# Performance work log

Hardware: AMD Instinct MI355X
Metric: run time of the kernel (lower is better)

## Reference

```python
import jax, jax.numpy as jnp
import numpy as np

T, N, E = 12, 100000, 3200000
F = H = 64
O, L = 32, 2


def setup_inputs() -> dict:
    key = jax.random.key(0)
    ks = jax.random.split(key, 13)
    sc = 0.08  # keep gate pre-activations in a sane range
    return {
        "x": jax.random.normal(ks[0], (T, N, F), jnp.float32),
        "hidden_states": jax.random.normal(ks[1], (L, N, H), jnp.float32),
        "cell_states": jax.random.normal(ks[2], (L, N, H), jnp.float32),
        "Wx_self": jax.random.normal(ks[3], (L, 4, F, H), jnp.float32) * sc,
        "Wx_neigh": jax.random.normal(ks[4], (L, 4, F, H), jnp.float32) * sc,
        "Wh_self": jax.random.normal(ks[5], (L, 4, H, H), jnp.float32) * sc,
        "Wh_neigh": jax.random.normal(ks[6], (L, 4, H, H), jnp.float32) * sc,
        "w_c": jax.random.normal(ks[7], (L, 3, H), jnp.float32) * sc,  # peephole i,f,o
        "bias": jax.random.normal(ks[8], (L, 4, H), jnp.float32) * sc,  # i,f,c,o
        "Wout": jax.random.normal(ks[9], (H, O), jnp.float32) * sc,
        "bout": jax.random.normal(ks[10], (O,), jnp.float32) * sc,
        "src": jax.random.randint(ks[11], (E,), 0, N, jnp.int32),
        "dst": jax.random.randint(ks[12], (E,), 0, N, jnp.int32),
    }


def reference(x, hidden_states, cell_states, Wx_self, Wx_neigh, Wh_self,
              Wh_neigh, w_c, bias, Wout, bout, src, dst):
    # mean aggregation over incoming edges (DGL copy_u + mean reduce)
    deg = jax.ops.segment_sum(jnp.ones((E,), x.dtype), dst, num_segments=N)
    deg_inv = jnp.where(deg > 0, 1.0 / deg, 0.0)[:, None]  # [N,1]

    def mean_agg(feat):  # [N,D] -> [N,D]
        return jax.ops.segment_sum(feat[src], dst, num_segments=N) * deg_inv

    def gates(feat, agg, Ws, Wn):  # Ws,Wn: [4,D,H] -> [4,N,H]
        return (jnp.einsum('nf,gfh->gnh', feat, Ws)
                + jnp.einsum('nf,gfh->gnh', agg, Wn))

    def step(carry, x_t):
        hs, cs = carry  # [L,N,H] each
        inp = x_t
        new_h, new_c = [], []
        for j in range(L):
            h, c = hs[j], cs[j]
            x_agg = mean_agg(inp)  # reuse_msg_passing: one agg shared by 4 gates
            h_agg = mean_agg(h)
            pre = gates(inp, x_agg, Wx_self[j], Wx_neigh[j]) \
                + gates(h, h_agg, Wh_self[j], Wh_neigh[j])  # [4,N,H]
            i = jax.nn.sigmoid(pre[0] + w_c[j, 0] * c + bias[j, 0])
            f = jax.nn.sigmoid(pre[1] + w_c[j, 1] * c + bias[j, 1])
            c_tilde = jnp.tanh(pre[2] + bias[j, 2])
            nc = f * c + i * c_tilde
            o = jax.nn.sigmoid(pre[3] + w_c[j, 2] * nc + bias[j, 3])
            nh = o * jnp.tanh(nc)
            new_h.append(nh)
            new_c.append(nc)
            inp = nh
        out_t = inp @ Wout + bout  # [N,O]
        return (jnp.stack(new_h), jnp.stack(new_c)), out_t

    (h_f, c_f), outs = jax.lax.scan(step, (hidden_states, cell_states), x)
    return outs, h_f, c_f  # outs: [T,N,O]
```

## Files before the change

### kernel.cpp

```cpp
#include <hip/hip_runtime.h>

#define T_STEPS 12
#define NN 100000
#define EE 3200000
#define HD 64
#define OD 32
#define NBK 391

typedef __attribute__((ext_vector_type(8))) short short8;
typedef __attribute__((ext_vector_type(4))) float f32x4;
typedef __attribute__((ext_vector_type(2))) float f32x2;
typedef unsigned short u16;
typedef unsigned char u8;

__device__ __forceinline__ u16 f2b(float x) {
  union { float f; unsigned u; } v; v.f = x;
  unsigned r = v.u + 0x7FFFu + ((v.u >> 16) & 1u);
  return (u16)(r >> 16);
}
__device__ __forceinline__ float sigm(float x) {
  x = fminf(fmaxf(x, -30.f), 30.f);
  return 1.0f / (1.0f + __expf(-x));
}
__device__ __forceinline__ float tanh_f(float x) {
  x = fminf(fmaxf(x, -15.f), 15.f);
  float e = __expf(2.0f * x);
  return (e - 1.0f) / (e + 1.0f);
}

__device__ __forceinline__ uint2 pack8_fp8(const float* f) {
  unsigned lo = 0, hi = 0;
  lo = __builtin_amdgcn_cvt_pk_fp8_f32(f[0], f[1], lo, false);
  lo = __builtin_amdgcn_cvt_pk_fp8_f32(f[2], f[3], lo, true);
  hi = __builtin_amdgcn_cvt_pk_fp8_f32(f[4], f[5], hi, false);
  hi = __builtin_amdgcn_cvt_pk_fp8_f32(f[6], f[7], hi, true);
  return make_uint2(lo, hi);
}
__device__ __forceinline__ u8 f2q(float x) {
  return (u8)(__builtin_amdgcn_cvt_pk_fp8_f32(x, 0.f, 0u, false) & 0xFFu);
}
__device__ __forceinline__ void acc8_fp8(uint2 v, float* a) {
  f32x2 p0 = __builtin_amdgcn_cvt_pk_f32_fp8(v.x, false);
  f32x2 p1 = __builtin_amdgcn_cvt_pk_f32_fp8(v.x, true);
  f32x2 p2 = __builtin_amdgcn_cvt_pk_f32_fp8(v.y, false);
  f32x2 p3 = __builtin_amdgcn_cvt_pk_f32_fp8(v.y, true);
  a[0] += p0[0]; a[1] += p0[1]; a[2] += p1[0]; a[3] += p1[1];
  a[4] += p2[0]; a[5] += p2[1]; a[6] += p3[0]; a[7] += p3[1];
}
__device__ __forceinline__ void dec16_acc(uint4 q, float* a) {
  f32x2 t;
  t = __builtin_amdgcn_cvt_pk_f32_fp8(q.x, false); a[0] += t[0]; a[1] += t[1];
  t = __builtin_amdgcn_cvt_pk_f32_fp8(q.x, true);  a[2] += t[0]; a[3] += t[1];
  t = __builtin_amdgcn_cvt_pk_f32_fp8(q.y, false); a[4] += t[0]; a[5] += t[1];
  t = __builtin_amdgcn_cvt_pk_f32_fp8(q.y, true);  a[6] += t[0]; a[7] += t[1];
  t = __builtin_amdgcn_cvt_pk_f32_fp8(q.z, false); a[8] += t[0]; a[9] += t[1];
  t = __builtin_amdgcn_cvt_pk_f32_fp8(q.z, true);  a[10] += t[0]; a[11] += t[1];
  t = __builtin_amdgcn_cvt_pk_f32_fp8(q.w, false); a[12] += t[0]; a[13] += t[1];
  t = __builtin_amdgcn_cvt_pk_f32_fp8(q.w, true);  a[14] += t[0]; a[15] += t[1];
}
__device__ __forceinline__ short8 s8_from_fp8(uint2 q) {
  f32x2 p0 = __builtin_amdgcn_cvt_pk_f32_fp8(q.x, false);
  f32x2 p1 = __builtin_amdgcn_cvt_pk_f32_fp8(q.x, true);
  f32x2 p2 = __builtin_amdgcn_cvt_pk_f32_fp8(q.y, false);
  f32x2 p3 = __builtin_amdgcn_cvt_pk_f32_fp8(q.y, true);
  short8 o;
  o[0] = (short)f2b(p0[0]); o[1] = (short)f2b(p0[1]);
  o[2] = (short)f2b(p1[0]); o[3] = (short)f2b(p1[1]);
  o[4] = (short)f2b(p2[0]); o[5] = (short)f2b(p2[1]);
  o[6] = (short)f2b(p3[0]); o[7] = (short)f2b(p3[1]);
  return o;
}
__device__ __forceinline__ short8 s8_from_f32(float4 a, float4 b) {
  short8 o;
  o[0] = (short)f2b(a.x); o[1] = (short)f2b(a.y);
  o[2] = (short)f2b(a.z); o[3] = (short)f2b(a.w);
  o[4] = (short)f2b(b.x); o[5] = (short)f2b(b.y);
  o[6] = (short)f2b(b.z); o[7] = (short)f2b(b.w);
  return o;
}

__global__ __launch_bounds__(256) void k_bhist(const int* __restrict__ dst,
                                               int* __restrict__ bcnt, int E) {
  __shared__ int h[NBK];
  for (int i = threadIdx.x; i < NBK; i += 256) h[i] = 0;
  __syncthreads();
  int base = blockIdx.x * 4096;
#pragma unroll
  for (int i = 0; i < 16; ++i) {
    int e = base + i * 256 + threadIdx.x;
    if (e < E) atomicAdd(&h[dst[e] >> 8], 1);
  }
  __syncthreads();
  for (int i = threadIdx.x; i < NBK; i += 256)
    if (h[i]) atomicAdd(&bcnt[i], h[i]);
}

__global__ __launch_bounds__(512) void k_bscan(const int* __restrict__ bcnt,
                                               int* __restrict__ bcur) {
  __shared__ int buf[512];
  int tid = threadIdx.x;
  int v = (tid < NBK) ? bcnt[tid] : 0;
  buf[tid] = v;
  __syncthreads();
  for (int off = 1; off < 512; off <<= 1) {
    int t = (tid >= off) ? buf[tid - off] : 0;
    __syncthreads();
    buf[tid] += t;
    __syncthreads();
  }
  if (tid < NBK) bcur[tid] = buf[tid] - v;
}

__global__ __launch_bounds__(256) void k_bscatter(const int* __restrict__ src,
                                                  const int* __restrict__ dst,
                                                  int* __restrict__ bcur,
                                                  uint2* __restrict__ binned, int E) {
  __shared__ int h[NBK];
  __shared__ int base[NBK];
  __shared__ int cur[NBK];
  for (int i = threadIdx.x; i < NBK; i += 256) { h[i] = 0; cur[i] = 0; }
  __syncthreads();
  int b0 = blockIdx.x * 4096;
  int d[16], s[16];
#pragma unroll
  for (int i = 0; i < 16; ++i) {
    int e = b0 + i * 256 + threadIdx.x;
    if (e < E) {
      d[i] = dst[e];
      s[i] = src[e];
      atomicAdd(&h[d[i] >> 8], 1);
    } else d[i] = -1;
  }
  __syncthreads();
  for (int i = threadIdx.x; i < NBK; i += 256)
    if (h[i]) base[i] = atomicAdd(&bcur[i], h[i]);
  __syncthreads();
#pragma unroll
  for (int i = 0; i < 16; ++i) {
    if (d[i] >= 0) {
      int bk = d[i] >> 8;
      int r = atomicAdd(&cur[bk], 1);
      binned[base[bk] + r] = make_uint2((unsigned)s[i], (unsigned)d[i]);
    }
  }
}

__global__ __launch_bounds__(256) void k_count2(const uint2* __restrict__ binned,
                                                int* __restrict__ deg, int E) {
  int e = blockIdx.x * 256 + threadIdx.x;
  if (e < E) atomicAdd(&deg[binned[e].y], 1);
}

__global__ __launch_bounds__(1024) void k_scanA(const int* __restrict__ deg,
                                                int* __restrict__ excl,
                                                int* __restrict__ btot, int n) {
  __shared__ int buf[1024];
  int tid = threadIdx.x;
  int i = blockIdx.x * 1024 + tid;
  int v = (i < n) ? deg[i] : 0;
  buf[tid] = v;
  __syncthreads();
  for (int off = 1; off < 1024; off <<= 1) {
    int t = (tid >= off) ? buf[tid - off] : 0;
    __syncthreads();
    buf[tid] += t;
    __syncthreads();
  }
  if (i < n) excl[i] = buf[tid] - v;
  if (tid == 1023) btot[blockIdx.x] = buf[1023];
}

__global__ __launch_bounds__(128) void k_scanB(const int* __restrict__ btot,
                                               int* __restrict__ boffs, int nb) {
  __shared__ int buf[128];
  int tid = threadIdx.x;
  int v = (tid < nb) ? btot[tid] : 0;
  buf[tid] = v;
  __syncthreads();
  for (int off = 1; off < 128; off <<= 1) {
    int t = (tid >= off) ? buf[tid - off] : 0;
    __syncthreads();
    buf[tid] += t;
    __syncthreads();
  }
  if (tid < nb) boffs[tid] = buf[tid] - v;
}

__global__ __launch_bounds__(1024) void k_scanC(const int* __restrict__ deg,
                                                const int* __restrict__ excl,
                                                const int* __restrict__ boffs,
                                                int* __restrict__ row_ptr,
                                                int* __restrict__ cursor,
                                                float* __restrict__ deg_inv, int n) {
  int i = blockIdx.x * 1024 + threadIdx.x;
  if (i < n) {
    int v = excl[i] + boffs[blockIdx.x];
    int d = deg[i];
    row_ptr[i] = v;
    cursor[i] = v;
    deg_inv[i] = d ? (1.0f / (float)d) : 0.0f;
    if (i == n - 1) row_ptr[n] = v + d;
  }
}

__global__ __launch_bounds__(256) void k_scatter2(const uint2* __restrict__ binned,
                                                  int* __restrict__ cursor,
                                                  int* __restrict__ csr, int E) {
  int e = blockIdx.x * 256 + threadIdx.x;
  if (e < E) {
    uint2 p = binned[e];
    int pos = atomicAdd(&cursor[p.y], 1);
    csr[pos] = (int)p.x;
  }
}

__global__ __launch_bounds__(256) void k_prep(const float* __restrict__ Wxs,
                                              const float* __restrict__ Wxn,
                                              const float* __restrict__ Whs,
                                              const float* __restrict__ Whn,
                                              u16* __restrict__ bprep) {
  int idx = blockIdx.x * 256 + threadIdx.x;
  int l = idx >> 16;
  int kb = (idx >> 13) & 7;
  int fi = (idx >> 9) & 15;
  int ln = (idx >> 3) & 63;
  int j = idx & 7;
  int fc = kb * 32 + ((ln >> 4) << 3) + j;
  int g = fi & 3;
  int kk = ((fi >> 2) << 4) + (ln & 15);
  int t = fc >> 6, f = fc & 63;
  const float* tabs[4] = {Wxs, Wxn, Whs, Whn};
  bprep[idx] = f2b(tabs[t][((size_t)(l * 4 + g) * 64 + f) * 64 + kk]);
}

__global__ __launch_bounds__(256) void k_prepw(const float* __restrict__ Wout,
                                               u16* __restrict__ wp) {
  int idx = blockIdx.x * 256 + threadIdx.x;
  int kb = idx >> 10;
  int fi = (idx >> 9) & 1;
  int ln = (idx >> 3) & 63;
  int j = idx & 7;
  int k = kb * 32 + ((ln >> 4) << 3) + j;
  int o = fi * 16 + (ln & 15);
  wp[idx] = f2b(Wout[k * 32 + o]);
}

__global__ __launch_bounds__(256) void k_convxall(const float* __restrict__ x,
                                                  u8* __restrict__ XQ) {
  int tid = blockIdx.x * 256 + threadIdx.x;
  int j = tid & 7;
  int tn = tid >> 3;
  int n = tn % NN;
  int t = tn / NN;
  const float* rp = x + (size_t)tn * 64 + j * 8;
  float4 v0 = *reinterpret_cast<const float4*>(rp);
  float4 v1 = *reinterpret_cast<const float4*>(rp + 4);
  float f[8] = {v0.x, v0.y, v0.z, v0.w, v1.x, v1.y, v1.z, v1.w};
  *reinterpret_cast<uint2*>(XQ + (size_t)n * 768 + t * 64 + j * 8) = pack8_fp8(f);
}

__global__ __launch_bounds__(256) void k_inith(const float* __restrict__ h0,
                                               u16* __restrict__ H0bf,
                                               u16* __restrict__ L1bf,
                                               u8* __restrict__ HQ) {
  int idx = blockIdx.x * 256 + threadIdx.x;
  int n = idx >> 3, j = idx & 7;
#pragma unroll
  for (int L = 0; L < 2; ++L) {
    const float* rp = h0 + (size_t)L * NN * 64 + (size_t)n * 64 + j * 8;
    float4 v0 = *reinterpret_cast<const float4*>(rp);
    float4 v1 = *reinterpret_cast<const float4*>(rp + 4);
    float f[8] = {v0.x, v0.y, v0.z, v0.w, v1.x, v1.y, v1.z, v1.w};
    short8 o;
#pragma unroll
    for (int i = 0; i < 8; ++i) o[i] = (short)f2b(f[i]);
    if (L == 0)
      *reinterpret_cast<short8*>(H0bf + (size_t)n * 64 + j * 8) = o;
    else
      *reinterpret_cast<short8*>(L1bf + (size_t)n * 64 + j * 8) = o;
    *reinterpret_cast<uint2*>(HQ + (size_t)n * 128 + L * 64 + j * 8) = pack8_fp8(f);
  }
}

__global__ __launch_bounds__(256) void k_aggx(const u8* __restrict__ XQ,
                                              const int* __restrict__ row_ptr,
                                              const int* __restrict__ csr,
                                              const float* __restrict__ deg_inv,
                                              u8* __restrict__ AGGXq) {
  int node = blockIdx.x * 4 + (threadIdx.x >> 6);
  int lane = threadIdx.x & 63;
  int g = lane >> 4, m = lane & 15;
  int start = row_ptr[node], end = row_ptr[node + 1];
  float acc[3][16];
#pragma unroll
  for (int p = 0; p < 3; ++p)
#pragma unroll
    for (int i = 0; i < 16; ++i) acc[p][i] = 0.f;
  int e = start + g;
  for (; e + 4 < end; e += 8) {
    int s0 = csr[e], s1 = csr[e + 4];
    const u8* r0 = XQ + (size_t)s0 * 768 + m * 16;
    const u8* r1 = XQ + (size_t)s1 * 768 + m * 16;
#pragma unroll
    for (int p = 0; p < 3; ++p) {
      uint4 q0 = *reinterpret_cast<const uint4*>(r0 + p * 256);
      uint4 q1 = *reinterpret_cast<const uint4*>(r1 + p * 256);
      dec16_acc(q0, acc[p]);
      dec16_acc(q1, acc[p]);
    }
  }
  if (e < end) {
    int s0 = csr[e];
    const u8* r0 = XQ + (size_t)s0 * 768 + m * 16;
#pragma unroll
    for (int p = 0; p < 3; ++p) {
      uint4 q0 = *reinterpret_cast<const uint4*>(r0 + p * 256);
      dec16_acc(q0, acc[p]);
    }
  }
#pragma unroll
  for (int off = 16; off < 64; off <<= 1)
#pragma unroll
    for (int p = 0; p < 3; ++p)
#pragma unroll
      for (int i = 0; i < 16; ++i) acc[p][i] += __shfl_xor(acc[p][i], off);
  if (g == 0) {
    float sc = deg_inv[node];
#pragma unroll
    for (int p = 0; p < 3; ++p) {
      float f[16];
#pragma unroll
      for (int i = 0; i < 16; ++i) f[i] = acc[p][i] * sc;
      uint4 o;
      unsigned w;
      w = 0; w = __builtin_amdgcn_cvt_pk_fp8_f32(f[0], f[1], w, false);
      w = __builtin_amdgcn_cvt_pk_fp8_f32(f[2], f[3], w, true); o.x = w;
      w = 0; w = __builtin_amdgcn_cvt_pk_fp8_f32(f[4], f[5], w, false);
      w = __builtin_amdgcn_cvt_pk_fp8_f32(f[6], f[7], w, true); o.y = w;
      w = 0; w = __builtin_amdgcn_cvt_pk_fp8_f32(f[8], f[9], w, false);
      w = __builtin_amdgcn_cvt_pk_fp8_f32(f[10], f[11], w, true); o.z = w;
      w = 0; w = __builtin_amdgcn_cvt_pk_fp8_f32(f[12], f[13], w, false);
      w = __builtin_amdgcn_cvt_pk_fp8_f32(f[14], f[15], w, true); o.w = w;
      int t = p * 4 + (m >> 2);
      *reinterpret_cast<uint4*>(AGGXq + ((size_t)t * NN + node) * 64 + (m & 3) * 16) = o;
    }
  }
}

__global__ __launch_bounds__(256) void k_agg_pair(const u8* __restrict__ Q,
                                                  const int* __restrict__ row_ptr,
                                                  const int* __restrict__ csr,
                                                  const float* __restrict__ deg_inv,
                                                  u16* __restrict__ outp) {
  int node = blockIdx.x * 4 + (threadIdx.x >> 6);
  int lane = threadIdx.x & 63;
  int g = lane >> 4, m = lane & 15;
  int start = row_ptr[node], end = row_ptr[node + 1];
  float a[8] = {0, 0, 0, 0, 0, 0, 0, 0};
  int e = start + g;
  for (; e + 12 < end; e += 16) {
    int s0 = csr[e], s1 = csr[e + 4], s2 = csr[e + 8], s3 = csr[e + 12];
    uint2 v0 = *reinterpret_cast<const uint2*>(Q + (size_t)s0 * 128 + m * 8);
    uint2 v1 = *reinterpret_cast<const uint2*>(Q + (size_t)s1 * 128 + m * 8);
    uint2 v2 = *reinterpret_cast<const uint2*>(Q + (size_t)s2 * 128 + m * 8);
    uint2 v3 = *reinterpret_cast<const uint2*>(Q + (size_t)s3 * 128 + m * 8);
    acc8_fp8(v0, a); acc8_fp8(v1, a); acc8_fp8(v2, a); acc8_fp8(v3, a);
  }
  if (e + 4 < end) {
    int s0 = csr[e], s1 = csr[e + 4];
    uint2 v0 = *reinterpret_cast<const uint2*>(Q + (size_t)s0 * 128 + m * 8);
    uint2 v1 = *reinterpret_cast<const uint2*>(Q + (size_t)s1 * 128 + m * 8);
    acc8_fp8(v0, a); acc8_fp8(v1, a);
    e += 8;
  }
  if (e < end) {
    int s0 = csr[e];
    uint2 v0 = *reinterpret_cast<const uint2*>(Q + (size_t)s0 * 128 + m * 8);
    acc8_fp8(v0, a);
  }
#pragma unroll
  for (int off = 16; off < 64; off <<= 1) {
#pragma unroll
    for (int i = 0; i < 8; ++i) a[i] += __shfl_xor(a[i], off);
  }
  if (g == 0) {
    float sc = deg_inv[node];
    short8 o;
#pragma unroll
    for (int i = 0; i < 8; ++i) o[i] = (short)f2b(a[i] * sc);
    *reinterpret_cast<short8*>(outp + (size_t)node * 128 + m * 8) = o;
  }
}

__global__ __launch_bounds__(256, 2) void k_gates0(
    const float* __restrict__ xin, const u8* __restrict__ aggxq,
    u16* __restrict__ h0bf, const u16* __restrict__ agghl,
    u8* __restrict__ hq, float* __restrict__ cst, float* __restrict__ hf32,
    const u16* __restrict__ bprepl,
    const float* __restrict__ wcl, const float* __restrict__ biasl,
    int n_nodes, int writef32) {
  const int tid = threadIdx.x;
  const int lane = tid & 63;
  const int w = tid >> 6;
  const int nb = blockIdx.x * 64;
  const int cl = lane & 15;
  const int kg = lane >> 4;

  short8 breg[8][4];
#pragma unroll
  for (int kb = 0; kb < 8; ++kb)
#pragma unroll
    for (int fl = 0; fl < 4; ++fl)
      breg[kb][fl] = *reinterpret_cast<const short8*>(
          bprepl + (kb << 13) + (((w << 2) + fl) << 9) + (lane << 3));

  int gnc[4];
#pragma unroll
  for (int rg = 0; rg < 4; ++rg) {
    int g = nb + rg * 16 + cl;
    gnc[rg] = (g < n_nodes) ? g : (n_nodes - 1);
  }

  f32x4 acc[4][4];
  f32x4 z4 = {0.f, 0.f, 0.f, 0.f};
#pragma unroll
  for (int a = 0; a < 4; ++a)
#pragma unroll
    for (int b = 0; b < 4; ++b) acc[a][b] = z4;

  const int koff = kg << 3;
#pragma unroll
  for (int kb = 0; kb < 8; ++kb) {
    const int idx = ((kb & 1) << 5) + koff;
#pragma unroll
    for (int rg = 0; rg < 4; ++rg) {
      short8 a;
      if (kb < 2) {
        const float* rp = xin + (size_t)gnc[rg] * 64 + idx;
        a = s8_from_f32(*reinterpret_cast<const float4*>(rp),
                        *reinterpret_cast<const float4*>(rp + 4));
      } else if (kb < 4) {
        a = s8_from_fp8(*reinterpret_cast<const uint2*>(aggxq + (size_t)gnc[rg] * 64 + idx));
      } else if (kb < 6) {
        a = *reinterpret_cast<const short8*>(h0bf + (size_t)gnc[rg] * 64 + idx);
      } else {
        a = *reinterpret_cast<const short8*>(agghl + (size_t)gnc[rg] * 128 + idx);
      }
      acc[rg][0] = __builtin_amdgcn_mfma_f32_16x16x32_bf16(a, breg[kb][0], acc[rg][0], 0, 0, 0);
      acc[rg][1] = __builtin_amdgcn_mfma_f32_16x16x32_bf16(a, breg[kb][1], acc[rg][1], 0, 0, 0);
      acc[rg][2] = __builtin_amdgcn_mfma_f32_16x16x32_bf16(a, breg[kb][2], acc[rg][2], 0, 0, 0);
      acc[rg][3] = __builtin_amdgcn_mfma_f32_16x16x32_bf16(a, breg[kb][3], acc[rg][3], 0, 0, 0);
    }
  }

  const int k = (w << 4) + cl;
  const float wci = wcl[k], wcf = wcl[64 + k], wco = wcl[128 + k];
  const float bi = biasl[k], bfg = biasl[64 + k], bc = biasl[128 + k], bo = biasl[192 + k];
#pragma unroll
  for (int rg = 0; rg < 4; ++rg) {
#pragma unroll
    for (int r = 0; r < 4; ++r) {
      int n = nb + rg * 16 + kg * 4 + r;
      if (n < n_nodes) {
        size_t off = (size_t)n * 64 + k;
        float c_old = cst[off];
        float ig = sigm(acc[rg][0][r] + wci * c_old + bi);
        float fg = sigm(acc[rg][1][r] + wcf * c_old + bfg);
        float ct = tanh_f(acc[rg][2][r] + bc);
        float nc = fg * c_old + ig * ct;
        float og = sigm(acc[rg][3][r] + wco * nc + bo);
        float nh = og * tanh_f(nc);
        cst[off] = nc;
        h0bf[off] = f2b(nh);
        hq[(size_t)n * 128 + k] = f2q(nh);
        if (writef32) hf32[off] = nh;
      }
    }
  }
}

__global__ __launch_bounds__(256, 2) void k_gates1(
    const u16* __restrict__ h0bf, const u16* __restrict__ agghl,
    u16* __restrict__ l1bf, u8* __restrict__ hq,
    float* __restrict__ cst, float* __restrict__ hf32,
    const u16* __restrict__ bprepl,
    const float* __restrict__ wcl, const float* __restrict__ biasl,
    const u16* __restrict__ wproj, const float* __restrict__ boutp,
    float* __restrict__ outp, int n_nodes, int writef32) {
  __shared__ u16 Hsm[64 * 64];
  const int tid = threadIdx.x;
  const int lane = tid & 63;
  const int w = tid >> 6;
  const int nb = blockIdx.x * 64;
  const int cl = lane & 15;
  const int kg = lane >> 4;

  short8 breg[8][4];
#pragma unroll
  for (int kb = 0; kb < 8; ++kb)
#pragma unroll
    for (int fl = 0; fl < 4; ++fl)
      breg[kb][fl] = *reinterpret_cast<const short8*>(
          bprepl + (kb << 13) + (((w << 2) + fl) << 9) + (lane << 3));

  int gnc[4];
#pragma unroll
  for (int rg = 0; rg < 4; ++rg) {
    int g = nb + rg * 16 + cl;
    gnc[rg] = (g < n_nodes) ? g : (n_nodes - 1);
  }

  f32x4 acc[4][4];
  f32x4 z4 = {0.f, 0.f, 0.f, 0.f};
#pragma unroll
  for (int a = 0; a < 4; ++a)
#pragma unroll
    for (int b = 0; b < 4; ++b) acc[a][b] = z4;

  const int koff = kg << 3;
#pragma unroll
  for (int kb = 0; kb < 8; ++kb) {
    const int idx = ((kb & 1) << 5) + koff;
#pragma unroll
    for (int rg = 0; rg < 4; ++rg) {
      short8 a;
      if (kb < 2) {
        a = *reinterpret_cast<const short8*>(h0bf + (size_t)gnc[rg] * 64 + idx);
      } else if (kb < 4) {
        a = *reinterpret_cast<const short8*>(agghl + (size_t)gnc[rg] * 128 + idx);
      } else if (kb < 6) {
        a = *reinterpret_cast<const short8*>(l1bf + (size_t)gnc[rg] * 64 + idx);
      } else {
        a = *reinterpret_cast<const short8*>(agghl + (size_t)gnc[rg] * 128 + 64 + idx);
      }
      acc[rg][0] = __builtin_amdgcn_mfma_f32_16x16x32_bf16(a, breg[kb][0], acc[rg][0], 0, 0, 0);
      acc[rg][1] = __builtin_amdgcn_mfma_f32_16x16x32_bf16(a, breg[kb][1], acc[rg][1], 0, 0, 0);
      acc[rg][2] = __builtin_amdgcn_mfma_f32_16x16x32_bf16(a, breg[kb][2], acc[rg][2], 0, 0, 0);
      acc[rg][3] = __builtin_amdgcn_mfma_f32_16x16x32_bf16(a, breg[kb][3], acc[rg][3], 0, 0, 0);
    }
  }

  const int k = (w << 4) + cl;
  const float wci = wcl[k], wcf = wcl[64 + k], wco = wcl[128 + k];
  const float bi = biasl[k], bfg = biasl[64 + k], bc = biasl[128 + k], bo = biasl[192 + k];
#pragma unroll
  for (int rg = 0; rg < 4; ++rg) {
#pragma unroll
    for (int r = 0; r < 4; ++r) {
      int n = nb + rg * 16 + kg * 4 + r;
      if (n < n_nodes) {
        size_t off = (size_t)n * 64 + k;
        float c_old = cst[off];
        float ig = sigm(acc[rg][0][r] + wci * c_old + bi);
        float fg = sigm(acc[rg][1][r] + wcf * c_old + bfg);
        float ct = tanh_f(acc[rg][2][r] + bc);
        float nc = fg * c_old + ig * ct;
        float og = sigm(acc[rg][3][r] + wco * nc + bo);
        float nh = og * tanh_f(nc);
        cst[off] = nc;
        u16 hb = f2b(nh);
        l1bf[off] = hb;
        hq[(size_t)n * 128 + 64 + k] = f2q(nh);
        Hsm[(rg * 16 + kg * 4 + r) * 64 + k] = hb;
        if (writef32) hf32[off] = nh;
      }
    }
  }

  __syncthreads();
  short8 bw[2][2];
#pragma unroll
  for (int kb = 0; kb < 2; ++kb)
#pragma unroll
    for (int fi = 0; fi < 2; ++fi)
      bw[kb][fi] = *reinterpret_cast<const short8*>(wproj + (((kb * 2 + fi) * 64 + lane) << 3));
  short8 a0 = *reinterpret_cast<const short8*>(&Hsm[(w * 16 + cl) * 64 + kg * 8]);
  short8 a1 = *reinterpret_cast<const short8*>(&Hsm[(w * 16 + cl) * 64 + 32 + kg * 8]);
  f32x4 p0 = z4, p1 = z4;
  p0 = __builtin_amdgcn_mfma_f32_16x16x32_bf16(a0, bw[0][0], p0, 0, 0, 0);
  p0 = __builtin_amdgcn_mfma_f32_16x16x32_bf16(a1, bw[1][0], p0, 0, 0, 0);
  p1 = __builtin_amdgcn_mfma_f32_16x16x32_bf16(a0, bw[0][1], p1, 0, 0, 0);
  p1 = __builtin_amdgcn_mfma_f32_16x16x32_bf16(a1, bw[1][1], p1, 0, 0, 0);
  const float bo0 = boutp[cl], bo1 = boutp[16 + cl];
#pragma unroll
  for (int r = 0; r < 4; ++r) {
    int n = nb + w * 16 + kg * 4 + r;
    if (n < n_nodes) {
      outp[(size_t)n * OD + cl] = p0[r] + bo0;
      outp[(size_t)n * OD + 16 + cl] = p1[r] + bo1;
    }
  }
}

extern "C" void kernel_launch(void* const* d_in, const int* in_sizes, int n_in,
                              void* d_out, int out_size, void* d_ws, size_t ws_size,
                              hipStream_t stream) {
  const float* x = (const float*)d_in[0];
  const float* h0 = (const float*)d_in[1];
  const float* c0 = (const float*)d_in[2];
  const float* Wxs = (const float*)d_in[3];
  const float* Wxn = (const float*)d_in[4];
  const float* Whs = (const float*)d_in[5];
  const float* Whn = (const float*)d_in[6];
  const float* wc = (const float*)d_in[7];
  const float* bias = (const float*)d_in[8];
  const float* Wout = (const float*)d_in[9];
  const float* bout = (const float*)d_in[10];
  const int* src = (const int*)d_in[11];
  const int* dst = (const int*)d_in[12];

  float* out = (float*)d_out;
  float* outs = out;
  float* hstate = out + (size_t)T_STEPS * NN * OD;
  float* cstate = hstate + (size_t)2 * NN * HD;

  char* p = (char*)d_ws;
  auto alloc = [&](size_t bytes) {
    char* r = p;
    p += (bytes + 255) & ~(size_t)255;
    return r;
  };
  int* csr = (int*)alloc((size_t)EE * 4);
  u8* XQ = (u8*)alloc((size_t)NN * 768);
  uint2* binned = (uint2*)XQ;
  u8* AGGXq = (u8*)alloc((size_t)T_STEPS * NN * 64);
  int* row_ptr = (int*)alloc((size_t)(NN + 1) * 4);
  int* cursor = (int*)alloc((size_t)NN * 4);
  int* deg = (int*)alloc((size_t)NN * 4);
  int* excl = (int*)alloc((size_t)NN * 4);
  int* btot = (int*)alloc(128 * 4);
  int* boffs = (int*)alloc(128 * 4);
  int* bcnt = (int*)alloc(NBK * 4);
  int* bcur = (int*)alloc(NBK * 4);
  float* deg_inv = (float*)alloc((size_t)NN * 4);
  u16* H0bf = (u16*)alloc((size_t)NN * 64 * 2);
  u16* L1bf = (u16*)alloc((size_t)NN * 64 * 2);
  u8* HQ = (u8*)alloc((size_t)NN * 128);
  u16* AGGHL = (u16*)alloc((size_t)NN * 128 * 2);
  u16* bprep = (u16*)alloc((size_t)2 * 65536 * 2);
  u16* wprep = (u16*)alloc((size_t)2048 * 2);

  const int nscan = (NN + 1023) / 1024;
  const int nchunk = (EE + 4095) / 4096;

  hipMemsetAsync(deg, 0, (size_t)NN * 4, stream);
  hipMemsetAsync(bcnt, 0, (size_t)NBK * 4, stream);
  k_bhist<<<nchunk, 256, 0, stream>>>(dst, bcnt, EE);
  k_bscan<<<1, 512, 0, stream>>>(bcnt, bcur);
  k_bscatter<<<nchunk, 256, 0, stream>>>(src, dst, bcur, binned, EE);
  k_count2<<<(EE + 255) / 256, 256, 0, stream>>>(binned, deg, EE);
  k_scanA<<<nscan, 1024, 0, stream>>>(deg, excl, btot, NN);
  k_scanB<<<1, 128, 0, stream>>>(btot, boffs, nscan);
  k_scanC<<<nscan, 1024, 0, stream>>>(deg, excl, boffs, row_ptr, cursor, deg_inv, NN);
  k_scatter2<<<(EE + 255) / 256, 256, 0, stream>>>(binned, cursor, csr, EE);
  k_prep<<<512, 256, 0, stream>>>(Wxs, Wxn, Whs, Whn, bprep);
  k_prepw<<<8, 256, 0, stream>>>(Wout, wprep);
  k_convxall<<<(T_STEPS * NN * 8 + 255) / 256, 256, 0, stream>>>(x, XQ);
  k_inith<<<NN * 8 / 256, 256, 0, stream>>>(h0, H0bf, L1bf, HQ);
  hipMemcpyAsync(cstate, c0, (size_t)2 * NN * HD * 4, hipMemcpyDeviceToDevice, stream);
  k_aggx<<<(NN + 3) / 4, 256, 0, stream>>>(XQ, row_ptr, csr, deg_inv, AGGXq);
  k_agg_pair<<<(NN + 3) / 4, 256, 0, stream>>>(HQ, row_ptr, csr, deg_inv, AGGHL);

  for (int t = 0; t < T_STEPS; ++t) {
    int wf = (t == T_STEPS - 1) ? 1 : 0;
    k_gates0<<<(NN + 63) / 64, 256, 0, stream>>>(
        x + (size_t)t * NN * HD, AGGXq + (size_t)t * NN * 64,
        H0bf, AGGHL, HQ, cstate, hstate, bprep, wc, bias, NN, wf);
    k_agg_pair<<<(NN + 3) / 4, 256, 0, stream>>>(HQ, row_ptr, csr, deg_inv, AGGHL);
    k_gates1<<<(NN + 63) / 64, 256, 0, stream>>>(
        H0bf, AGGHL, L1bf, HQ,
        cstate + (size_t)NN * HD, hstate + (size_t)NN * HD,
        bprep + 65536, wc + 192, bias + 256,
        wprep, bout, outs + (size_t)t * NN * OD, NN, wf);
  }
}
```

Before: 2.998 ms.

## Fuse layer-1 gates with next step's layer-0 gates; widen aggregation loads

Layer-1 gates for step t and layer-0 gates for step t+1 now run in one kernel, after a single pairwise aggregation per step. Layer 0 of step 0 is hoisted before the loop. This saves a launch per step, and the second half rereads the block's own h0 and aggregate rows while they are likely still cached. The pair-aggregation kernel now uses 16-byte fp8 loads with 8 lanes per row and packed f32x2 accumulation, to cut gather instruction count. The cost is higher register pressure in the fused kernel and extra barriers for shared-memory reuse.

```diff
diff --git a/kernel.cpp b/kernel.cpp
--- a/kernel.cpp
+++ b/kernel.cpp
@@ -39,24 +39,15 @@
 __device__ __forceinline__ u8 f2q(float x) {
   return (u8)(__builtin_amdgcn_cvt_pk_fp8_f32(x, 0.f, 0u, false) & 0xFFu);
 }
-__device__ __forceinline__ void acc8_fp8(uint2 v, float* a) {
-  f32x2 p0 = __builtin_amdgcn_cvt_pk_f32_fp8(v.x, false);
-  f32x2 p1 = __builtin_amdgcn_cvt_pk_f32_fp8(v.x, true);
-  f32x2 p2 = __builtin_amdgcn_cvt_pk_f32_fp8(v.y, false);
-  f32x2 p3 = __builtin_amdgcn_cvt_pk_f32_fp8(v.y, true);
-  a[0] += p0[0]; a[1] += p0[1]; a[2] += p1[0]; a[3] += p1[1];
-  a[4] += p2[0]; a[5] += p2[1]; a[6] += p3[0]; a[7] += p3[1];
-}
-__device__ __forceinline__ void dec16_acc(uint4 q, float* a) {
-  f32x2 t;
-  t = __builtin_amdgcn_cvt_pk_f32_fp8(q.x, false); a[0] += t[0]; a[1] += t[1];
-  t = __builtin_amdgcn_cvt_pk_f32_fp8(q.x, true);  a[2] += t[0]; a[3] += t[1];
-  t = __builtin_amdgcn_cvt_pk_f32_fp8(q.y, false); a[4] += t[0]; a[5] += t[1];
-  t = __builtin_amdgcn_cvt_pk_f32_fp8(q.y, true);  a[6] += t[0]; a[7] += t[1];
-  t = __builtin_amdgcn_cvt_pk_f32_fp8(q.z, false); a[8] += t[0]; a[9] += t[1];
-  t = __builtin_amdgcn_cvt_pk_f32_fp8(q.z, true);  a[10] += t[0]; a[11] += t[1];
-  t = __builtin_amdgcn_cvt_pk_f32_fp8(q.w, false); a[12] += t[0]; a[13] += t[1];
-  t = __builtin_amdgcn_cvt_pk_f32_fp8(q.w, true);  a[14] += t[0]; a[15] += t[1];
+__device__ __forceinline__ void dec16_acc2(uint4 q, f32x2* a) {
+  a[0] += __builtin_amdgcn_cvt_pk_f32_fp8(q.x, false);
+  a[1] += __builtin_amdgcn_cvt_pk_f32_fp8(q.x, true);
+  a[2] += __builtin_amdgcn_cvt_pk_f32_fp8(q.y, false);
+  a[3] += __builtin_amdgcn_cvt_pk_f32_fp8(q.y, true);
+  a[4] += __builtin_amdgcn_cvt_pk_f32_fp8(q.z, false);
+  a[5] += __builtin_amdgcn_cvt_pk_f32_fp8(q.z, true);
+  a[6] += __builtin_amdgcn_cvt_pk_f32_fp8(q.w, false);
+  a[7] += __builtin_amdgcn_cvt_pk_f32_fp8(q.w, true);
 }
 __device__ __forceinline__ short8 s8_from_fp8(uint2 q) {
   f32x2 p0 = __builtin_amdgcn_cvt_pk_f32_fp8(q.x, false);
@@ -291,11 +282,11 @@
   int lane = threadIdx.x & 63;
   int g = lane >> 4, m = lane & 15;
   int start = row_ptr[node], end = row_ptr[node + 1];
-  float acc[3][16];
+  f32x2 acc[3][8];
 #pragma unroll
   for (int p = 0; p < 3; ++p)
 #pragma unroll
-    for (int i = 0; i < 16; ++i) acc[p][i] = 0.f;
+    for (int i = 0; i < 8; ++i) acc[p][i] = (f32x2){0.f, 0.f};
   int e = start + g;
   for (; e + 4 < end; e += 8) {
     int s0 = csr[e], s1 = csr[e + 4];
@@ -305,8 +296,8 @@
     for (int p = 0; p < 3; ++p) {
       uint4 q0 = *reinterpret_cast<const uint4*>(r0 + p * 256);
       uint4 q1 = *reinterpret_cast<const uint4*>(r1 + p * 256);
-      dec16_acc(q0, acc[p]);
-      dec16_acc(q1, acc[p]);
+      dec16_acc2(q0, acc[p]);
+      dec16_acc2(q1, acc[p]);
     }
   }
   if (e < end) {
@@ -315,7 +306,7 @@
 #pragma unroll
     for (int p = 0; p < 3; ++p) {
       uint4 q0 = *reinterpret_cast<const uint4*>(r0 + p * 256);
-      dec16_acc(q0, acc[p]);
+      dec16_acc2(q0, acc[p]);
     }
   }
 #pragma unroll
@@ -323,14 +314,20 @@
 #pragma unroll
     for (int p = 0; p < 3; ++p)
 #pragma unroll
-      for (int i = 0; i < 16; ++i) acc[p][i] += __shfl_xor(acc[p][i], off);
+      for (int i = 0; i < 8; ++i) {
+        acc[p][i][0] += __shfl_xor(acc[p][i][0], off);
+        acc[p][i][1] += __shfl_xor(acc[p][i][1], off);
+      }
   if (g == 0) {
     float sc = deg_inv[node];
 #pragma unroll
     for (int p = 0; p < 3; ++p) {
       float f[16];
 #pragma unroll
-      for (int i = 0; i < 16; ++i) f[i] = acc[p][i] * sc;
+      for (int i = 0; i < 8; ++i) {
+        f[i * 2] = acc[p][i][0] * sc;
+        f[i * 2 + 1] = acc[p][i][1] * sc;
+      }
       uint4 o;
       unsigned w;
       w = 0; w = __builtin_amdgcn_cvt_pk_fp8_f32(f[0], f[1], w, false);
@@ -354,41 +351,51 @@
                                                   u16* __restrict__ outp) {
   int node = blockIdx.x * 4 + (threadIdx.x >> 6);
   int lane = threadIdx.x & 63;
-  int g = lane >> 4, m = lane & 15;
+  int g = lane >> 3, m = lane & 7;
   int start = row_ptr[node], end = row_ptr[node + 1];
-  float a[8] = {0, 0, 0, 0, 0, 0, 0, 0};
+  f32x2 a[8];
+#pragma unroll
+  for (int i = 0; i < 8; ++i) a[i] = (f32x2){0.f, 0.f};
   int e = start + g;
-  for (; e + 12 < end; e += 16) {
-    int s0 = csr[e], s1 = csr[e + 4], s2 = csr[e + 8], s3 = csr[e + 12];
-    uint2 v0 = *reinterpret_cast<const uint2*>(Q + (size_t)s0 * 128 + m * 8);
-    uint2 v1 = *reinterpret_cast<const uint2*>(Q + (size_t)s1 * 128 + m * 8);
-    uint2 v2 = *reinterpret_cast<const uint2*>(Q + (size_t)s2 * 128 + m * 8);
-    uint2 v3 = *reinterpret_cast<const uint2*>(Q + (size_t)s3 * 128 + m * 8);
-    acc8_fp8(v0, a); acc8_fp8(v1, a); acc8_fp8(v2, a); acc8_fp8(v3, a);
-  }
-  if (e + 4 < end) {
-    int s0 = csr[e], s1 = csr[e + 4];
-    uint2 v0 = *reinterpret_cast<const uint2*>(Q + (size_t)s0 * 128 + m * 8);
-    uint2 v1 = *reinterpret_cast<const uint2*>(Q + (size_t)s1 * 128 + m * 8);
-    acc8_fp8(v0, a); acc8_fp8(v1, a);
-    e += 8;
+  for (; e + 24 < end; e += 32) {
+    int s0 = csr[e], s1 = csr[e + 8], s2 = csr[e + 16], s3 = csr[e + 24];
+    uint4 q0 = *reinterpret_cast<const uint4*>(Q + (size_t)s0 * 128 + m * 16);
+    uint4 q1 = *reinterpret_cast<const uint4*>(Q + (size_t)s1 * 128 + m * 16);
+    uint4 q2 = *reinterpret_cast<const uint4*>(Q + (size_t)s2 * 128 + m * 16);
+    uint4 q3 = *reinterpret_cast<const uint4*>(Q + (size_t)s3 * 128 + m * 16);
+    dec16_acc2(q0, a); dec16_acc2(q1, a); dec16_acc2(q2, a); dec16_acc2(q3, a);
+  }
+  if (e + 8 < end) {
+    int s0 = csr[e], s1 = csr[e + 8];
+    uint4 q0 = *reinterpret_cast<const uint4*>(Q + (size_t)s0 * 128 + m * 16);
+    uint4 q1 = *reinterpret_cast<const uint4*>(Q + (size_t)s1 * 128 + m * 16);
+    dec16_acc2(q0, a); dec16_acc2(q1, a);
+    e += 16;
   }
   if (e < end) {
     int s0 = csr[e];
-    uint2 v0 = *reinterpret_cast<const uint2*>(Q + (size_t)s0 * 128 + m * 8);
-    acc8_fp8(v0, a);
-  }
-#pragma unroll
-  for (int off = 16; off < 64; off <<= 1) {
-#pragma unroll
-    for (int i = 0; i < 8; ++i) a[i] += __shfl_xor(a[i], off);
-  }
+    uint4 q0 = *reinterpret_cast<const uint4*>(Q + (size_t)s0 * 128 + m * 16);
+    dec16_acc2(q0, a);
+  }
+#pragma unroll
+  for (int off = 8; off < 64; off <<= 1)
+#pragma unroll
+    for (int i = 0; i < 8; ++i) {
+      a[i][0] += __shfl_xor(a[i][0], off);
+      a[i][1] += __shfl_xor(a[i][1], off);
+    }
   if (g == 0) {
     float sc = deg_inv[node];
-    short8 o;
-#pragma unroll
-    for (int i = 0; i < 8; ++i) o[i] = (short)f2b(a[i] * sc);
-    *reinterpret_cast<short8*>(outp + (size_t)node * 128 + m * 8) = o;
+    short8 o0, o1;
+#pragma unroll
+    for (int i = 0; i < 4; ++i) {
+      o0[i * 2] = (short)f2b(a[i][0] * sc);
+      o0[i * 2 + 1] = (short)f2b(a[i][1] * sc);
+      o1[i * 2] = (short)f2b(a[4 + i][0] * sc);
+      o1[i * 2 + 1] = (short)f2b(a[4 + i][1] * sc);
+    }
+    *reinterpret_cast<short8*>(outp + (size_t)node * 128 + m * 16) = o0;
+    *reinterpret_cast<short8*>(outp + (size_t)node * 128 + m * 16 + 8) = o1;
   }
 }
 
@@ -452,6 +459,7 @@
       acc[rg][3] = __builtin_amdgcn_mfma_f32_16x16x32_bf16(a, breg[kb][3], acc[rg][3], 0, 0, 0);
     }
   }
+  __syncthreads();
 
   const int k = (w << 4) + cl;
   const float wci = wcl[k], wcf = wcl[64 + k], wco = wcl[128 + k];
@@ -479,14 +487,16 @@
   }
 }
 
-__global__ __launch_bounds__(256, 2) void k_gates1(
-    const u16* __restrict__ h0bf, const u16* __restrict__ agghl,
+__global__ __launch_bounds__(256, 2) void k_gates10(
+    u16* __restrict__ h0bf, const u16* __restrict__ agghl,
     u16* __restrict__ l1bf, u8* __restrict__ hq,
     float* __restrict__ cst, float* __restrict__ hf32,
-    const u16* __restrict__ bprepl,
-    const float* __restrict__ wcl, const float* __restrict__ biasl,
+    const u16* __restrict__ bprep0, const u16* __restrict__ bprep1,
+    const float* __restrict__ wc, const float* __restrict__ bias,
     const u16* __restrict__ wproj, const float* __restrict__ boutp,
-    float* __restrict__ outp, int n_nodes, int writef32) {
+    float* __restrict__ outp,
+    const float* __restrict__ xnext, const u8* __restrict__ aggxqnext,
+    int n_nodes, int do0, int wf0, int wf1) {
   __shared__ u16 Hsm[64 * 64];
   const int tid = threadIdx.x;
   const int lane = tid & 63;
@@ -494,14 +504,9 @@
   const int nb = blockIdx.x * 64;
   const int cl = lane & 15;
   const int kg = lane >> 4;
-
-  short8 breg[8][4];
-#pragma unroll
-  for (int kb = 0; kb < 8; ++kb)
-#pragma unroll
-    for (int fl = 0; fl < 4; ++fl)
-      breg[kb][fl] = *reinterpret_cast<const short8*>(
-          bprepl + (kb << 13) + (((w << 2) + fl) << 9) + (lane << 3));
+  const int koff = kg << 3;
+  const int k = (w << 4) + cl;
+  f32x4 z4 = {0.f, 0.f, 0.f, 0.f};
 
   int gnc[4];
 #pragma unroll
@@ -510,84 +515,160 @@
     gnc[rg] = (g < n_nodes) ? g : (n_nodes - 1);
   }
 
-  f32x4 acc[4][4];
-  f32x4 z4 = {0.f, 0.f, 0.f, 0.f};
-#pragma unroll
-  for (int a = 0; a < 4; ++a)
-#pragma unroll
-    for (int b = 0; b < 4; ++b) acc[a][b] = z4;
-
-  const int koff = kg << 3;
-#pragma unroll
-  for (int kb = 0; kb < 8; ++kb) {
-    const int idx = ((kb & 1) << 5) + koff;
+  {
+    short8 breg[8][4];
+#pragma unroll
+    for (int kb = 0; kb < 8; ++kb)
+#pragma unroll
+      for (int fl = 0; fl < 4; ++fl)
+        breg[kb][fl] = *reinterpret_cast<const short8*>(
+            bprep1 + (kb << 13) + (((w << 2) + fl) << 9) + (lane << 3));
+
+    f32x4 acc[4][4];
+#pragma unroll
+    for (int a = 0; a < 4; ++a)
+#pragma unroll
+      for (int b = 0; b < 4; ++b) acc[a][b] = z4;
+
+#pragma unroll
+    for (int kb = 0; kb < 8; ++kb) {
+      const int idx = ((kb & 1) << 5) + koff;
+#pragma unroll
+      for (int rg = 0; rg < 4; ++rg) {
+        short8 a;
+        if (kb < 2) {
+          a = *reinterpret_cast<const short8*>(h0bf + (size_t)gnc[rg] * 64 + idx);
+        } else if (kb < 4) {
+          a = *reinterpret_cast<const short8*>(agghl + (size_t)gnc[rg] * 128 + idx);
+        } else if (kb < 6) {
+          a = *reinterpret_cast<const short8*>(l1bf + (size_t)gnc[rg] * 64 + idx);
+        } else {
+          a = *reinterpret_cast<const short8*>(agghl + (size_t)gnc[rg] * 128 + 64 + idx);
+        }
+        acc[rg][0] = __builtin_amdgcn_mfma_f32_16x16x32_bf16(a, breg[kb][0], acc[rg][0], 0, 0, 0);
+        acc[rg][1] = __builtin_amdgcn_mfma_f32_16x16x32_bf16(a, breg[kb][1], acc[rg][1], 0, 0, 0);
+        acc[rg][2] = __builtin_amdgcn_mfma_f32_16x16x32_bf16(a, breg[kb][2], acc[rg][2], 0, 0, 0);
+        acc[rg][3] = __builtin_amdgcn_mfma_f32_16x16x32_bf16(a, breg[kb][3], acc[rg][3], 0, 0, 0);
+      }
+    }
+    __syncthreads();
+
+    float* cst1 = cst + (size_t)NN * 64;
+    const float wci = wc[192 + k], wcf = wc[256 + k], wco = wc[320 + k];
+    const float bi = bias[256 + k], bfg = bias[320 + k], bc = bias[384 + k], bo = bias[448 + k];
 #pragma unroll
     for (int rg = 0; rg < 4; ++rg) {
-      short8 a;
-      if (kb < 2) {
-        a = *reinterpret_cast<const short8*>(h0bf + (size_t)gnc[rg] * 64 + idx);
-      } else if (kb < 4) {
-        a = *reinterpret_cast<const short8*>(agghl + (size_t)gnc[rg] * 128 + idx);
-      } else if (kb < 6) {
-        a = *reinterpret_cast<const short8*>(l1bf + (size_t)gnc[rg] * 64 + idx);
-      } else {
-        a = *reinterpret_cast<const short8*>(agghl + (size_t)gnc[rg] * 128 + 64 + idx);
-      }
-      acc[rg][0] = __builtin_amdgcn_mfma_f32_16x16x32_bf16(a, breg[kb][0], acc[rg][0], 0, 0, 0);
-      acc[rg][1] = __builtin_amdgcn_mfma_f32_16x16x32_bf16(a, breg[kb][1], acc[rg][1], 0, 0, 0);
-      acc[rg][2] = __builtin_amdgcn_mfma_f32_16x16x32_bf16(a, breg[kb][2], acc[rg][2], 0, 0, 0);
-      acc[rg][3] = __builtin_amdgcn_mfma_f32_16x16x32_bf16(a, breg[kb][3], acc[rg][3], 0, 0, 0);
-    }
-  }
-
-  const int k = (w << 4) + cl;
-  const float wci = wcl[k], wcf = wcl[64 + k], wco = wcl[128 + k];
-  const float bi = biasl[k], bfg = biasl[64 + k], bc = biasl[128 + k], bo = biasl[192 + k];
-#pragma unroll
-  for (int rg = 0; rg < 4; ++rg) {
+#pragma unroll
+      for (int r = 0; r < 4; ++r) {
+        int n = nb + rg * 16 + kg * 4 + r;
+        if (n < n_nodes) {
+          size_t off = (size_t)n * 64 + k;
+          float c_old = cst1[off];
+          float ig = sigm(acc[rg][0][r] + wci * c_old + bi);
+          float fg = sigm(acc[rg][1][r] + wcf * c_old + bfg);
+          float ct = tanh_f(acc[rg][2][r] + bc);
+          float nc = fg * c_old + ig * ct;
+          float og = sigm(acc[rg][3][r] + wco * nc + bo);
+          float nh = og * tanh_f(nc);
+          cst1[off] = nc;
+          u16 hb = f2b(nh);
+          l1bf[off] = hb;
+          hq[(size_t)n * 128 + 64 + k] = f2q(nh);
+          Hsm[(rg * 16 + kg * 4 + r) * 64 + k] = hb;
+          if (wf1) hf32[(size_t)NN * 64 + off] = nh;
+        }
+      }
+    }
+  }
+
+  __syncthreads();
+  {
+    short8 bw[2][2];
+#pragma unroll
+    for (int kb = 0; kb < 2; ++kb)
+#pragma unroll
+      for (int fi = 0; fi < 2; ++fi)
+        bw[kb][fi] = *reinterpret_cast<const short8*>(wproj + (((kb * 2 + fi) * 64 + lane) << 3));
+    short8 a0 = *reinterpret_cast<const short8*>(&Hsm[(w * 16 + cl) * 64 + kg * 8]);
+    short8 a1 = *reinterpret_cast<const short8*>(&Hsm[(w * 16 + cl) * 64 + 32 + kg * 8]);
+    f32x4 p0 = z4, p1 = z4;
+    p0 = __builtin_amdgcn_mfma_f32_16x16x32_bf16(a0, bw[0][0], p0, 0, 0, 0);
+    p0 = __builtin_amdgcn_mfma_f32_16x16x32_bf16(a1, bw[1][0], p0, 0, 0, 0);
+    p1 = __builtin_amdgcn_mfma_f32_16x16x32_bf16(a0, bw[0][1], p1, 0, 0, 0);
+    p1 = __builtin_amdgcn_mfma_f32_16x16x32_bf16(a1, bw[1][1], p1, 0, 0, 0);
+    const float bo0 = boutp[cl], bo1 = boutp[16 + cl];
 #pragma unroll
     for (int r = 0; r < 4; ++r) {
-      int n = nb + rg * 16 + kg * 4 + r;
+      int n = nb + w * 16 + kg * 4 + r;
       if (n < n_nodes) {
-        size_t off = (size_t)n * 64 + k;
-        float c_old = cst[off];
-        float ig = sigm(acc[rg][0][r] + wci * c_old + bi);
-        float fg = sigm(acc[rg][1][r] + wcf * c_old + bfg);
-        float ct = tanh_f(acc[rg][2][r] + bc);
-        float nc = fg * c_old + ig * ct;
-        float og = sigm(acc[rg][3][r] + wco * nc + bo);
-        float nh = og * tanh_f(nc);
-        cst[off] = nc;
-        u16 hb = f2b(nh);
-        l1bf[off] = hb;
-        hq[(size_t)n * 128 + 64 + k] = f2q(nh);
-        Hsm[(rg * 16 + kg * 4 + r) * 64 + k] = hb;
-        if (writef32) hf32[off] = nh;
-      }
-    }
-  }
-
-  __syncthreads();
-  short8 bw[2][2];
-#pragma unroll
-  for (int kb = 0; kb < 2; ++kb)
-#pragma unroll
-    for (int fi = 0; fi < 2; ++fi)
-      bw[kb][fi] = *reinterpret_cast<const short8*>(wproj + (((kb * 2 + fi) * 64 + lane) << 3));
-  short8 a0 = *reinterpret_cast<const short8*>(&Hsm[(w * 16 + cl) * 64 + kg * 8]);
-  short8 a1 = *reinterpret_cast<const short8*>(&Hsm[(w * 16 + cl) * 64 + 32 + kg * 8]);
-  f32x4 p0 = z4, p1 = z4;
-  p0 = __builtin_amdgcn_mfma_f32_16x16x32_bf16(a0, bw[0][0], p0, 0, 0, 0);
-  p0 = __builtin_amdgcn_mfma_f32_16x16x32_bf16(a1, bw[1][0], p0, 0, 0, 0);
-  p1 = __builtin_amdgcn_mfma_f32_16x16x32_bf16(a0, bw[0][1], p1, 0, 0, 0);
-  p1 = __builtin_amdgcn_mfma_f32_16x16x32_bf16(a1, bw[1][1], p1, 0, 0, 0);
-  const float bo0 = boutp[cl], bo1 = boutp[16 + cl];
-#pragma unroll
-  for (int r = 0; r < 4; ++r) {
-    int n = nb + w * 16 + kg * 4 + r;
-    if (n < n_nodes) {
-      outp[(size_t)n * OD + cl] = p0[r] + bo0;
-      outp[(size_t)n * OD + 16 + cl] = p1[r] + bo1;
+        outp[(size_t)n * OD + cl] = p0[r] + bo0;
+        outp[(size_t)n * OD + 16 + cl] = p1[r] + bo1;
+      }
+    }
+  }
+
+  if (do0) {
+    short8 breg[8][4];
+#pragma unroll
+    for (int kb = 0; kb < 8; ++kb)
+#pragma unroll
+      for (int fl = 0; fl < 4; ++fl)
+        breg[kb][fl] = *reinterpret_cast<const short8*>(
+            bprep0 + (kb << 13) + (((w << 2) + fl) << 9) + (lane << 3));
+
+    f32x4 acc[4][4];
+#pragma unroll
+    for (int a = 0; a < 4; ++a)
+#pragma unroll
+      for (int b = 0; b < 4; ++b) acc[a][b] = z4;
+
+#pragma unroll
+    for (int kb = 0; kb < 8; ++kb) {
+      const int idx = ((kb & 1) << 5) + koff;
+#pragma unroll
+      for (int rg = 0; rg < 4; ++rg) {
+        short8 a;
+        if (kb < 2) {
+          const float* rp = xnext + (size_t)gnc[rg] * 64 + idx;
+          a = s8_from_f32(*reinterpret_cast<const float4*>(rp),
+                          *reinterpret_cast<const float4*>(rp + 4));
+        } else if (kb < 4) {
+          a = s8_from_fp8(*reinterpret_cast<const uint2*>(aggxqnext + (size_t)gnc[rg] * 64 + idx));
+        } else if (kb < 6) {
+          a = *reinterpret_cast<const short8*>(h0bf + (size_t)gnc[rg] * 64 + idx);
+        } else {
+          a = *reinterpret_cast<const short8*>(agghl + (size_t)gnc[rg] * 128 + idx);
+        }
+        acc[rg][0] = __builtin_amdgcn_mfma_f32_16x16x32_bf16(a, breg[kb][0], acc[rg][0], 0, 0, 0);
+        acc[rg][1] = __builtin_amdgcn_mfma_f32_16x16x32_bf16(a, breg[kb][1], acc[rg][1], 0, 0, 0);
+        acc[rg][2] = __builtin_amdgcn_mfma_f32_16x16x32_bf16(a, breg[kb][2], acc[rg][2], 0, 0, 0);
+        acc[rg][3] = __builtin_amdgcn_mfma_f32_16x16x32_bf16(a, breg[kb][3], acc[rg][3], 0, 0, 0);
+      }
+    }
+    __syncthreads();
+
+    const float wci = wc[k], wcf = wc[64 + k], wco = wc[128 + k];
+    const float bi = bias[k], bfg = bias[64 + k], bc = bias[128 + k], bo = bias[192 + k];
+#pragma unroll
+    for (int rg = 0; rg < 4; ++rg) {
+#pragma unroll
+      for (int r = 0; r < 4; ++r) {
+        int n = nb + rg * 16 + kg * 4 + r;
+        if (n < n_nodes) {
+          size_t off = (size_t)n * 64 + k;
+          float c_old = cst[off];
+          float ig = sigm(acc[rg][0][r] + wci * c_old + bi);
+          float fg = sigm(acc[rg][1][r] + wcf * c_old + bfg);
+          float ct = tanh_f(acc[rg][2][r] + bc);
+          float nc = fg * c_old + ig * ct;
+          float og = sigm(acc[rg][3][r] + wco * nc + bo);
+          float nh = og * tanh_f(nc);
+          cst[off] = nc;
+          h0bf[off] = f2b(nh);
+          hq[(size_t)n * 128 + k] = f2q(nh);
+          if (wf0) hf32[off] = nh;
+        }
+      }
     }
   }
 }
@@ -661,16 +742,20 @@
   k_aggx<<<(NN + 3) / 4, 256, 0, stream>>>(XQ, row_ptr, csr, deg_inv, AGGXq);
   k_agg_pair<<<(NN + 3) / 4, 256, 0, stream>>>(HQ, row_ptr, csr, deg_inv, AGGHL);
 
+  k_gates0<<<(NN + 63) / 64, 256, 0, stream>>>(
+      x, AGGXq, H0bf, AGGHL, HQ, cstate, hstate, bprep, wc, bias, NN, 0);
+
   for (int t = 0; t < T_STEPS; ++t) {
-    int wf = (t == T_STEPS - 1) ? 1 : 0;
-    k_gates0<<<(NN + 63) / 64, 256, 0, stream>>>(
-        x + (size_t)t * NN * HD, AGGXq + (size_t)t * NN * 64,
-        H0bf, AGGHL, HQ, cstate, hstate, bprep, wc, bias, NN, wf);
+    int do0 = (t < T_STEPS - 1) ? 1 : 0;
+    int wf0 = (t == T_STEPS - 2) ? 1 : 0;
+    int wf1 = (t == T_STEPS - 1) ? 1 : 0;
     k_agg_pair<<<(NN + 3) / 4, 256, 0, stream>>>(HQ, row_ptr, csr, deg_inv, AGGHL);
-    k_gates1<<<(NN + 63) / 64, 256, 0, stream>>>(
-        H0bf, AGGHL, L1bf, HQ,
-        cstate + (size_t)NN * HD, hstate + (size_t)NN * HD,
-        bprep + 65536, wc + 192, bias + 256,
-        wprep, bout, outs + (size_t)t * NN * OD, NN, wf);
-  }
-}
+    const float* xn = do0 ? (x + (size_t)(t + 1) * NN * HD) : x;
+    const u8* an = do0 ? (AGGXq + (size_t)(t + 1) * NN * 64) : AGGXq;
+    k_gates10<<<(NN + 63) / 64, 256, 0, stream>>>(
+        H0bf, AGGHL, L1bf, HQ, cstate, hstate,
+        bprep, bprep + 65536, wc, bias,
+        wprep, bout, outs + (size_t)t * NN * OD,
+        xn, an, NN, do0, wf0, wf1);
+  }
+}
```

Result: slower. 3.534 ms (+17.9%).
